# Optimization experiments

Hardware: AMD Instinct MI355X
Metric: run time of the kernel (lower is better)

The kernel has to match this reference:

```python
import jax, jax.numpy as jnp
import numpy as np

VOCAB = 100000
SHORTLIST = 10000  # cutoffs = [10000, 20000, 40000, 80000], n_clusters = 4
B, T, D = 1024, 128, 1024


def setup_inputs() -> dict:
    key = jax.random.key(0)
    ks = jax.random.split(key, 12)
    s = 0.02  # realistic init scale for weights
    inp = {
        "features": jax.random.normal(ks[0], (B, D), jnp.float32),
        "head_weight": jax.random.normal(ks[1], (SHORTLIST + 4, D), jnp.float32) * s,
        "proj0": jax.random.normal(ks[2], (512, D), jnp.float32) * s,
        "out0": jax.random.normal(ks[3], (10000, 512), jnp.float32) * s,
        "proj1": jax.random.normal(ks[4], (256, D), jnp.float32) * s,
        "out1": jax.random.normal(ks[5], (20000, 256), jnp.float32) * s,
        "proj2": jax.random.normal(ks[6], (128, D), jnp.float32) * s,
        "out2": jax.random.normal(ks[7], (40000, 128), jnp.float32) * s,
        "proj3": jax.random.normal(ks[8], (64, D), jnp.float32) * s,
        "out3": jax.random.normal(ks[9], (20000, 64), jnp.float32) * s,
        "discard_probs": jax.random.uniform(ks[10], (VOCAB,), jnp.float32),
        "targets": jax.random.randint(ks[11], (B, T), 0, VOCAB, jnp.int64),
        "target_mask": jnp.ones((B, T), jnp.bool_),
    }
    return inp


def _adaptive_log_prob(x, head_weight, projs, outs):
    # head: shortlist logits + one logit per tail cluster
    head_lp = jax.nn.log_softmax(x @ head_weight.T, axis=-1)  # [B, SHORTLIST+4]
    parts = [head_lp[:, :SHORTLIST]]
    for i, (pw, ow) in enumerate(zip(projs, outs)):
        cluster_logits = (x @ pw.T) @ ow.T  # [B, osz]
        parts.append(jax.nn.log_softmax(cluster_logits, axis=-1)
                     + head_lp[:, SHORTLIST + i:SHORTLIST + i + 1])
    return jnp.concatenate(parts, axis=-1)  # [B, VOCAB]


def reference(features, head_weight, proj0, out0, proj1, out1, proj2, out2,
              proj3, out3, discard_probs, targets, target_mask):
    # dropout is identity in eval/reference mode
    logprob = _adaptive_log_prob(features, head_weight,
                                 (proj0, proj1, proj2, proj3),
                                 (out0, out1, out2, out3))
    lp_t = jnp.take_along_axis(logprob, targets, axis=1)        # [B, T]
    w = (1.0 - discard_probs[targets]) * target_mask.astype(lp_t.dtype)
    per_sample = jnp.sum(-lp_t * w, axis=1) / jnp.sum(w, axis=1)  # [B]
    return jnp.sum(per_sample) / (targets.shape[0] + 1e-5)
```

## Files before the change

kernel.cpp:

```cpp
#include <hip/hip_runtime.h>
#include <cstdint>


typedef unsigned short u16;
typedef __attribute__((ext_vector_type(4))) float f32x4;
typedef __attribute__((ext_vector_type(8))) __bf16 bf16x8;
typedef __attribute__((ext_vector_type(4))) unsigned int u32x4;

__device__ __forceinline__ u16 f2bf(float f){
  unsigned u = __float_as_uint(f);
  u += 0x7FFFu + ((u >> 16) & 1u);
  return (u16)(u >> 16);
}

__device__ __forceinline__ void load_lds16(const void* g, void* l){
  __builtin_amdgcn_global_load_lds(
      (__attribute__((address_space(1))) void*)(uintptr_t)g,
      (__attribute__((address_space(3))) void*)(unsigned)(uintptr_t)l,
      16, 0, 0);
}

__device__ __forceinline__ float wave_sum(float v){
  #pragma unroll
  for (int d = 1; d < 64; d <<= 1) v += __shfl_xor(v, d, 64);
  return v;
}

__device__ __forceinline__ float wave_dot(const u16* a, const u16* b, int len, int lane){
  float s = 0.f;
  for (int k = lane*8; k < len; k += 512){
    u32x4 va = *(const u32x4*)(a + k);
    u32x4 vb = *(const u32x4*)(b + k);
    #pragma unroll
    for (int i = 0; i < 4; i++){
      unsigned ua = va[i], ub = vb[i];
      s = fmaf(__uint_as_float(ua << 16),        __uint_as_float(ub << 16),        s);
      s = fmaf(__uint_as_float(ua & 0xFFFF0000u), __uint_as_float(ub & 0xFFFF0000u), s);
    }
  }
  return wave_sum(s);
}

struct CvtSeg { const float* src; u16* dst; unsigned start; };
struct CvtTab { CvtSeg s[10]; unsigned total; };

__global__ __launch_bounds__(256) void cvt_bf16(CvtTab t){
  unsigned stride = gridDim.x * blockDim.x;
  for (unsigned c = blockIdx.x*blockDim.x + threadIdx.x; c < t.total; c += stride){
    int si = 0;
    #pragma unroll
    for (int i = 1; i < 10; i++) if (c >= t.s[i].start) si = i;
    unsigned lo = c - t.s[si].start;
    const float4* sp = (const float4*)t.s[si].src + (size_t)lo*2;
    float4 f0 = sp[0], f1 = sp[1];
    uint4 d;
    d.x = (unsigned)f2bf(f0.x) | ((unsigned)f2bf(f0.y) << 16);
    d.y = (unsigned)f2bf(f0.z) | ((unsigned)f2bf(f0.w) << 16);
    d.z = (unsigned)f2bf(f1.x) | ((unsigned)f2bf(f1.y) << 16);
    d.w = (unsigned)f2bf(f1.z) | ((unsigned)f2bf(f1.w) << 16);
    ((uint4*)t.s[si].dst)[lo] = d;
  }
}

struct GemmSeg {
  const u16* A; const u16* B; float* part; u16* C; float* gates;
  int lda, N, K, ntiles, tileStart, ldc;
};
struct GemmTab { GemmSeg seg[5]; int nseg; };

__global__ __launch_bounds__(256) void gemm_ms(GemmTab tab){
  __shared__ u16 ldsA[128*64];
  __shared__ u16 ldsB[128*64];
  __shared__ float msLds[128][2];

  int bx = blockIdx.y;
  int s = 0;
  #pragma unroll
  for (int i = 1; i < 5; i++)
    if (i < tab.nseg && bx >= tab.seg[i].tileStart) s = i;
  const u16* Ab = tab.seg[s].A;
  const u16* Bb = tab.seg[s].B;
  float* part = tab.seg[s].part;
  u16* Cc = tab.seg[s].C;
  float* gatesp = tab.seg[s].gates;
  int lda = tab.seg[s].lda, N = tab.seg[s].N, K = tab.seg[s].K;
  int ntiles = tab.seg[s].ntiles, ldc = tab.seg[s].ldc;
  int tileN = bx - tab.seg[s].tileStart;
  int row0 = blockIdx.x * 128;
  int n0 = tileN * 128;

  int tid = threadIdx.x;
  int wid = tid >> 6, lane = tid & 63;
  int wr = wid >> 1, wc = wid & 1;
  int qr = lane >> 4, ln = lane & 15;

  f32x4 acc[4][4];
  const f32x4 zero = {0.f, 0.f, 0.f, 0.f};
  #pragma unroll
  for (int i = 0; i < 4; i++)
    #pragma unroll
    for (int j = 0; j < 4; j++) acc[i][j] = zero;

  int rr_[4], kcs_[4];
  #pragma unroll
  for (int j = 0; j < 4; j++){
    int c = (wid*4 + j)*64 + lane;
    rr_[j]  = c >> 3;
    kcs_[j] = (c & 7) ^ (rr_[j] & 7);
  }

  int nkt = K >> 6;
  for (int kt = 0; kt < nkt; kt++){
    int kbase = kt * 64;
    #pragma unroll
    for (int j = 0; j < 4; j++){
      const u16* g = Ab + (size_t)(row0 + rr_[j])*lda + kbase + kcs_[j]*8;
      load_lds16(g, (char*)ldsA + (size_t)(wid*4 + j)*1024);
    }
    #pragma unroll
    for (int j = 0; j < 4; j++){
      int nr = n0 + rr_[j]; if (nr >= N) nr = N - 1;
      const u16* g = Bb + (size_t)nr*K + kbase + kcs_[j]*8;
      load_lds16(g, (char*)ldsB + (size_t)(wid*4 + j)*1024);
    }
    __syncthreads();
    #pragma unroll
    for (int ks = 0; ks < 2; ks++){
      bf16x8 av[4], bv[4];
      #pragma unroll
      for (int mt = 0; mt < 4; mt++){
        int rl = wr*64 + mt*16 + ln;
        int ch = rl*8 + ((ks*4 + qr) ^ (rl & 7));
        av[mt] = *(const bf16x8*)((const char*)ldsA + ch*16);
      }
      #pragma unroll
      for (int nt = 0; nt < 4; nt++){
        int rl = wc*64 + nt*16 + ln;
        int ch = rl*8 + ((ks*4 + qr) ^ (rl & 7));
        bv[nt] = *(const bf16x8*)((const char*)ldsB + ch*16);
      }
      #pragma unroll
      for (int mt = 0; mt < 4; mt++)
        #pragma unroll
        for (int nt = 0; nt < 4; nt++)
          acc[mt][nt] = __builtin_amdgcn_mfma_f32_16x16x32_bf16(av[mt], bv[nt], acc[mt][nt], 0, 0, 0);
    }
    __syncthreads();
  }

  if (part){
    #pragma unroll
    for (int mt = 0; mt < 4; mt++){
      #pragma unroll
      for (int r = 0; r < 4; r++){
        float ss = 0.f;
        #pragma unroll
        for (int nt = 0; nt < 4; nt++){
          int col = n0 + wc*64 + nt*16 + ln;
          if (col < N){
            float v = acc[mt][nt][r];
            ss += __expf(v);
            if (gatesp && col >= 10000){
              int row = row0 + wr*64 + mt*16 + qr*4 + r;
              gatesp[row*4 + (col - 10000)] = v;
            }
          }
        }
        ss += __shfl_xor(ss, 1, 64);
        ss += __shfl_xor(ss, 2, 64);
        ss += __shfl_xor(ss, 4, 64);
        ss += __shfl_xor(ss, 8, 64);
        if (ln == 0) msLds[wr*64 + mt*16 + qr*4 + r][wc] = ss;
      }
    }
    __syncthreads();
    if (tid < 128)
      part[(size_t)(row0 + tid)*ntiles + tileN] = msLds[tid][0] + msLds[tid][1];
  } else {
    #pragma unroll
    for (int mt = 0; mt < 4; mt++)
      #pragma unroll
      for (int nt = 0; nt < 4; nt++)
        #pragma unroll
        for (int r = 0; r < 4; r++){
          int col = n0 + wc*64 + nt*16 + ln;
          if (col < N){
            int row = row0 + wr*64 + mt*16 + qr*4 + r;
            Cc[(size_t)row*ldc + col] = f2bf(acc[mt][nt][r]);
          }
        }
  }
}

template<int K, int MLOOP>
__global__ __launch_bounds__(256) void gemm_bres(const u16* __restrict__ A,
    const u16* __restrict__ B, float* __restrict__ part,
    int lda, int N, int ntiles){
  constexpr int KC = K/8;
  __shared__ u16 ldsB[128*K];
  __shared__ u16 ldsA[128*64];
  float* msLds = (float*)ldsA;

  int tid = threadIdx.x;
  int wid = tid >> 6, lane = tid & 63;
  int wr = wid >> 1, wc = wid & 1;
  int qr = lane >> 4, ln = lane & 15;
  int tileN = blockIdx.x;
  int n0 = tileN * 128;

  #pragma unroll
  for (int j = 0; j < KC/2; j++){
    int p = (wid*(KC/2) + j)*64 + lane;
    int row = p / KC;
    int jj  = p % KC;
    int nr = n0 + row; if (nr >= N) nr = N - 1;
    const u16* g = B + (size_t)nr*K + (size_t)(jj ^ (row & 7))*8;
    load_lds16(g, (char*)ldsB + (size_t)(wid*(KC/2) + j)*1024);
  }

  for (int m = 0; m < MLOOP; m++){
    int mbase = (blockIdx.y*MLOOP + m)*128;
    f32x4 acc[4][4];
    const f32x4 zero = {0.f, 0.f, 0.f, 0.f};
    #pragma unroll
    for (int i = 0; i < 4; i++)
      #pragma unroll
      for (int j = 0; j < 4; j++) acc[i][j] = zero;

    #pragma unroll
    for (int kt = 0; kt < K/64; kt++){
      #pragma unroll
      for (int j = 0; j < 4; j++){
        int p = (wid*4 + j)*64 + lane;
        int row = p >> 3, jj = p & 7;
        const u16* g = A + (size_t)(mbase + row)*lda + kt*64 + (jj ^ (row & 7))*8;
        load_lds16(g, (char*)ldsA + (size_t)(wid*4 + j)*1024);
      }
      __syncthreads();
      #pragma unroll
      for (int ks = 0; ks < 2; ks++){
        bf16x8 av[4], bv[4];
        #pragma unroll
        for (int mt = 0; mt < 4; mt++){
          int rl = wr*64 + mt*16 + ln;
          int ch = rl*8 + ((ks*4 + qr) ^ (rl & 7));
          av[mt] = *(const bf16x8*)((const char*)ldsA + ch*16);
        }
        #pragma unroll
        for (int nt = 0; nt < 4; nt++){
          int rl = wc*64 + nt*16 + ln;
          int kg = kt*8 + ks*4 + qr;
          int ch = rl*KC + (kg ^ (rl & 7));
          bv[nt] = *(const bf16x8*)((const char*)ldsB + ch*16);
        }
        #pragma unroll
        for (int mt = 0; mt < 4; mt++)
          #pragma unroll
          for (int nt = 0; nt < 4; nt++)
            acc[mt][nt] = __builtin_amdgcn_mfma_f32_16x16x32_bf16(av[mt], bv[nt], acc[mt][nt], 0, 0, 0);
      }
      __syncthreads();
    }

    #pragma unroll
    for (int mt = 0; mt < 4; mt++){
      #pragma unroll
      for (int r = 0; r < 4; r++){
        float ss = 0.f;
        #pragma unroll
        for (int nt = 0; nt < 4; nt++){
          int col = n0 + wc*64 + nt*16 + ln;
          if (col < N) ss += __expf(acc[mt][nt][r]);
        }
        ss += __shfl_xor(ss, 1, 64);
        ss += __shfl_xor(ss, 2, 64);
        ss += __shfl_xor(ss, 4, 64);
        ss += __shfl_xor(ss, 8, 64);
        if (ln == 0) msLds[(wr*64 + mt*16 + qr*4 + r)*2 + wc] = ss;
      }
    }
    __syncthreads();
    if (tid < 128)
      part[(size_t)(mbase + tid)*ntiles + tileN] = msLds[tid*2] + msLds[tid*2 + 1];
    __syncthreads();
  }
}

struct LseTab { const float* base[5]; int ntiles[5]; float* lse; };

__global__ __launch_bounds__(256) void lse_reduce(LseTab t){
  int widx = blockIdx.x*4 + (threadIdx.x >> 6);
  int lane = threadIdx.x & 63;
  int mat = widx >> 10, row = widx & 1023;
  const float* p = t.base[mat] + (size_t)row * t.ntiles[mat];
  float s = 0.f;
  for (int i = lane; i < t.ntiles[mat]; i += 64) s += p[i];
  s = wave_sum(s);
  if (lane == 0) t.lse[mat*1024 + row] = __logf(s);
}

struct GatherArgs {
  const u16* Xb; const u16* Hb; const u16* Hact; const u16* Ob;
  const float* lse; const float* gates; const int* targets; float* lp;
};

__global__ __launch_bounds__(256) void gather_k(GatherArgs g){
  int idx = blockIdx.x*4 + (threadIdx.x >> 6);
  int lane = threadIdx.x & 63;
  int v = g.targets[idx];
  int b = idx >> 7;
  float val;
  if (v < 10000){
    float logit = wave_dot(g.Xb + (size_t)b*1024, g.Hb + (size_t)v*1024, 1024, lane);
    val = logit - g.lse[b];
  } else {
    int c, off, psz, hoff; size_t oboff;
    if      (v < 20000){ c=0; off=10000; psz=512; hoff=0;   oboff=0; }
    else if (v < 40000){ c=1; off=20000; psz=256; hoff=512; oboff=5120000; }
    else if (v < 80000){ c=2; off=40000; psz=128; hoff=768; oboff=10240000; }
    else               { c=3; off=80000; psz=64;  hoff=896; oboff=15360000; }
    float logit = wave_dot(g.Hact + (size_t)b*960 + hoff,
                           g.Ob + oboff + (size_t)(v - off)*psz, psz, lane);
    val = g.gates[b*4 + c] - g.lse[b] + logit - g.lse[(c+1)*1024 + b];
  }
  if (lane == 0) g.lp[idx] = val;
}

__global__ __launch_bounds__(128) void row_loss(const float* lp, const int* targets,
                                                const float* discard, float* psamp){
  int b = blockIdx.x, t = threadIdx.x;
  int idx = b*128 + t;
  int v = targets[idx];
  float w = 1.0f - discard[v];
  float a = -lp[idx] * w;
  float as = wave_sum(a), ws = wave_sum(w);
  __shared__ float sa[2], sw[2];
  int wid = t >> 6, lane = t & 63;
  if (lane == 0){ sa[wid] = as; sw[wid] = ws; }
  __syncthreads();
  if (t == 0) psamp[b] = (sa[0] + sa[1]) / (sw[0] + sw[1]);
}

__global__ __launch_bounds__(256) void final_sum(const float* psamp, float* out){
  float s = 0.f;
  for (int i = threadIdx.x; i < 1024; i += 256) s += psamp[i];
  s = wave_sum(s);
  __shared__ float sb[4];
  if ((threadIdx.x & 63) == 0) sb[threadIdx.x >> 6] = s;
  __syncthreads();
  if (threadIdx.x == 0) out[0] = (sb[0] + sb[1] + sb[2] + sb[3]) / (1024.0f + 1e-5f);
}

extern "C" void kernel_launch(void* const* d_in, const int* in_sizes, int n_in,
                              void* d_out, int out_size, void* d_ws, size_t ws_size,
                              hipStream_t stream){
  (void)in_sizes; (void)n_in; (void)out_size; (void)ws_size;
  const float* features = (const float*)d_in[0];
  const float* head_w   = (const float*)d_in[1];
  const float* proj[4]  = {(const float*)d_in[2], (const float*)d_in[4],
                           (const float*)d_in[6], (const float*)d_in[8]};
  const float* outw[4]  = {(const float*)d_in[3], (const float*)d_in[5],
                           (const float*)d_in[7], (const float*)d_in[9]};
  const float* discard  = (const float*)d_in[10];
  const int*   targets  = (const int*)d_in[11];
  float* out = (float*)d_out;

  char* wsp = (char*)d_ws;
  size_t off = 0;
  auto carve = [&](size_t bytes)->char*{
    char* p = wsp + off; off += (bytes + 255) & ~(size_t)255; return p;
  };
  u16* Xb     = (u16*)carve(1024ull*1024*2);
  u16* Hb     = (u16*)carve(10004ull*1024*2);
  u16* Pb     = (u16*)carve(960ull*1024*2);
  u16* Ob     = (u16*)carve(16640000ull*2);
  u16* Hact   = (u16*)carve(1024ull*960*2);
  float* part = (float*)carve(803840ull*4);
  float* lse  = (float*)carve(5*1024*4);
  float* gates= (float*)carve(4096*4);
  float* lp   = (float*)carve(131072ull*4);
  float* psamp= (float*)carve(1024*4);

  CvtTab ct{};
  const float* srcs[10] = {features, head_w, proj[0], proj[1], proj[2], proj[3],
                           outw[0], outw[1], outw[2], outw[3]};
  u16* dsts[10] = {Xb, Hb, Pb, Pb + 512*1024, Pb + 768*1024, Pb + 896*1024,
                   Ob, Ob + 5120000, Ob + 10240000, Ob + 15360000};
  unsigned counts[10] = {1048576u, 10244096u, 524288u, 262144u, 131072u, 65536u,
                         5120000u, 5120000u, 5120000u, 1280000u};
  unsigned pre = 0;
  for (int i = 0; i < 10; i++){
    ct.s[i].src = srcs[i]; ct.s[i].dst = dsts[i]; ct.s[i].start = pre;
    pre += counts[i] / 8;
  }
  ct.total = pre;
  cvt_bf16<<<dim3(4096), dim3(256), 0, stream>>>(ct);

  float* pHead = part;
  float* pC0 = part + 80896;
  float* pC1 = part + 161792;
  float* pC2 = part + 322560;
  float* pC3 = part + 643072;

  GemmTab t1{};
  t1.nseg = 5;
  t1.seg[0] = {Xb, Hb,            pHead,   nullptr,    gates,   1024, 10004, 1024, 79, 0,  0};
  t1.seg[1] = {Xb, Pb,            nullptr, Hact,       nullptr, 1024, 512,   1024, 4,  79, 960};
  t1.seg[2] = {Xb, Pb + 512*1024, nullptr, Hact + 512, nullptr, 1024, 256,   1024, 2,  83, 960};
  t1.seg[3] = {Xb, Pb + 768*1024, nullptr, Hact + 768, nullptr, 1024, 128,   1024, 1,  85, 960};
  t1.seg[4] = {Xb, Pb + 896*1024, nullptr, Hact + 896, nullptr, 1024, 64,    1024, 1,  86, 960};
  gemm_ms<<<dim3(8, 87), dim3(256), 0, stream>>>(t1);

  GemmTab t2{};
  t2.nseg = 1;
  t2.seg[0] = {Hact, Ob, pC0, nullptr, nullptr, 960, 10000, 512, 79, 0, 0};
  gemm_ms<<<dim3(8, 79), dim3(256), 0, stream>>>(t2);

  gemm_bres<256,2><<<dim3(157, 4), dim3(256), 0, stream>>>(
      Hact + 512, Ob + 5120000, pC1, 960, 20000, 157);
  gemm_bres<128,2><<<dim3(313, 4), dim3(256), 0, stream>>>(
      Hact + 768, Ob + 10240000, pC2, 960, 40000, 313);
  gemm_bres<64,2><<<dim3(157, 4), dim3(256), 0, stream>>>(
      Hact + 896, Ob + 15360000, pC3, 960, 20000, 157);

  LseTab lt{};
  lt.base[0] = pHead; lt.base[1] = pC0; lt.base[2] = pC1; lt.base[3] = pC2; lt.base[4] = pC3;
  lt.ntiles[0] = 79; lt.ntiles[1] = 79; lt.ntiles[2] = 157; lt.ntiles[3] = 313; lt.ntiles[4] = 157;
  lt.lse = lse;
  lse_reduce<<<dim3(1280), dim3(256), 0, stream>>>(lt);

  GatherArgs ga{Xb, Hb, Hact, Ob, lse, gates, targets, lp};
  gather_k<<<dim3(32768), dim3(256), 0, stream>>>(ga);

  row_loss<<<dim3(1024), dim3(128), 0, stream>>>(lp, targets, discard, psamp);
  final_sum<<<dim3(1), dim3(256), 0, stream>>>(psamp, out);
}
```

Before: 361.3 us.

## Replace gemm_ms with register-prefetched 256x128 tile GEMM for head and cluster0

The multi-segment GEMM now uses 256x128 tiles, with each wave owning 64 rows across all 128 columns. Global loads for the next K step are prefetched into registers while MFMAs run on the current LDS tile, replacing the synchronous global_load_lds path. The larger tile halves the number of row blocks and cuts reloads of B. It also drops the cross-wave LDS reduction, so each wave writes its partial sum directly. The cost is more registers (a 4x8 accumulator plus prefetch buffers, with launch bounds of 2), fewer blocks in the grid, and a wider epilogue.

```diff
diff --git a/kernel.cpp b/kernel.cpp
--- a/kernel.cpp
+++ b/kernel.cpp
@@ -62,90 +62,98 @@
   }
 }
 
-struct GemmSeg {
-  const u16* A; const u16* B; float* part; u16* C; float* gates;
-  int lda, N, K, ntiles, tileStart, ldc;
-};
-struct GemmTab { GemmSeg seg[5]; int nseg; };
-
-__global__ __launch_bounds__(256) void gemm_ms(GemmTab tab){
-  __shared__ u16 ldsA[128*64];
+struct PSeg { const u16* B; float* part; u16* C; float* gates;
+              int N, K, ntiles, tileStart, ldc; };
+struct PTab { const u16* A; int lda; PSeg seg[5]; int nseg; };
+
+__global__ __launch_bounds__(256, 2) void gemm_pipe(PTab tab){
+  __shared__ u16 ldsA[256*64];
   __shared__ u16 ldsB[128*64];
-  __shared__ float msLds[128][2];
-
-  int bx = blockIdx.y;
+
+  int by = blockIdx.y;
   int s = 0;
   #pragma unroll
   for (int i = 1; i < 5; i++)
-    if (i < tab.nseg && bx >= tab.seg[i].tileStart) s = i;
-  const u16* Ab = tab.seg[s].A;
+    if (i < tab.nseg && by >= tab.seg[i].tileStart) s = i;
   const u16* Bb = tab.seg[s].B;
-  float* part = tab.seg[s].part;
-  u16* Cc = tab.seg[s].C;
+  float* part   = tab.seg[s].part;
+  u16* Cc       = tab.seg[s].C;
   float* gatesp = tab.seg[s].gates;
-  int lda = tab.seg[s].lda, N = tab.seg[s].N, K = tab.seg[s].K;
+  int N = tab.seg[s].N, K = tab.seg[s].K;
   int ntiles = tab.seg[s].ntiles, ldc = tab.seg[s].ldc;
-  int tileN = bx - tab.seg[s].tileStart;
-  int row0 = blockIdx.x * 128;
+  int tileN = by - tab.seg[s].tileStart;
   int n0 = tileN * 128;
+  int row0 = blockIdx.x * 256;
+  int lda = tab.lda;
 
   int tid = threadIdx.x;
-  int wid = tid >> 6, lane = tid & 63;
-  int wr = wid >> 1, wc = wid & 1;
+  int w = tid >> 6, lane = tid & 63;
   int qr = lane >> 4, ln = lane & 15;
 
-  f32x4 acc[4][4];
+  const char* baseA = (const char*)(tab.A + (size_t)row0*lda);
+  const char* baseB = (const char*)Bb;
+  unsigned offA[8], offB[4];
+  #pragma unroll
+  for (int t = 0; t < 8; t++){
+    int c = t*256 + tid, row = c >> 3, jj = (c & 7) ^ (row & 7);
+    offA[t] = (unsigned)(row*lda + jj*8) * 2u;
+  }
+  #pragma unroll
+  for (int t = 0; t < 4; t++){
+    int c = t*256 + tid, row = c >> 3, jj = (c & 7) ^ (row & 7);
+    int nr = n0 + row; if (nr >= N) nr = N - 1;
+    offB[t] = (unsigned)(nr*K + jj*8) * 2u;
+  }
+
+  u32x4 pa[8], pb[4];
+  #pragma unroll
+  for (int t = 0; t < 8; t++) pa[t] = *(const u32x4*)(baseA + offA[t]);
+  #pragma unroll
+  for (int t = 0; t < 4; t++) pb[t] = *(const u32x4*)(baseB + offB[t]);
+
+  f32x4 acc[4][8];
   const f32x4 zero = {0.f, 0.f, 0.f, 0.f};
   #pragma unroll
   for (int i = 0; i < 4; i++)
     #pragma unroll
-    for (int j = 0; j < 4; j++) acc[i][j] = zero;
-
-  int rr_[4], kcs_[4];
-  #pragma unroll
-  for (int j = 0; j < 4; j++){
-    int c = (wid*4 + j)*64 + lane;
-    rr_[j]  = c >> 3;
-    kcs_[j] = (c & 7) ^ (rr_[j] & 7);
-  }
+    for (int j = 0; j < 8; j++) acc[i][j] = zero;
 
   int nkt = K >> 6;
   for (int kt = 0; kt < nkt; kt++){
-    int kbase = kt * 64;
-    #pragma unroll
-    for (int j = 0; j < 4; j++){
-      const u16* g = Ab + (size_t)(row0 + rr_[j])*lda + kbase + kcs_[j]*8;
-      load_lds16(g, (char*)ldsA + (size_t)(wid*4 + j)*1024);
-    }
-    #pragma unroll
-    for (int j = 0; j < 4; j++){
-      int nr = n0 + rr_[j]; if (nr >= N) nr = N - 1;
-      const u16* g = Bb + (size_t)nr*K + kbase + kcs_[j]*8;
-      load_lds16(g, (char*)ldsB + (size_t)(wid*4 + j)*1024);
-    }
     __syncthreads();
     #pragma unroll
+    for (int t = 0; t < 8; t++)
+      *(u32x4*)((char*)ldsA + (size_t)(t*256 + tid)*16) = pa[t];
+    #pragma unroll
+    for (int t = 0; t < 4; t++)
+      *(u32x4*)((char*)ldsB + (size_t)(t*256 + tid)*16) = pb[t];
+    __syncthreads();
+    if (kt + 1 < nkt){
+      unsigned kb = (unsigned)(kt + 1) * 128u;
+      #pragma unroll
+      for (int t = 0; t < 8; t++) pa[t] = *(const u32x4*)(baseA + offA[t] + kb);
+      #pragma unroll
+      for (int t = 0; t < 4; t++) pb[t] = *(const u32x4*)(baseB + offB[t] + kb);
+    }
+    #pragma unroll
     for (int ks = 0; ks < 2; ks++){
-      bf16x8 av[4], bv[4];
+      bf16x8 av[4];
       #pragma unroll
       for (int mt = 0; mt < 4; mt++){
-        int rl = wr*64 + mt*16 + ln;
+        int rl = w*64 + mt*16 + ln;
         int ch = rl*8 + ((ks*4 + qr) ^ (rl & 7));
         av[mt] = *(const bf16x8*)((const char*)ldsA + ch*16);
       }
       #pragma unroll
-      for (int nt = 0; nt < 4; nt++){
-        int rl = wc*64 + nt*16 + ln;
+      for (int nt = 0; nt < 8; nt++){
+        int rl = nt*16 + ln;
         int ch = rl*8 + ((ks*4 + qr) ^ (rl & 7));
-        bv[nt] = *(const bf16x8*)((const char*)ldsB + ch*16);
-      }
-      #pragma unroll
-      for (int mt = 0; mt < 4; mt++)
-        #pragma unroll
-        for (int nt = 0; nt < 4; nt++)
-          acc[mt][nt] = __builtin_amdgcn_mfma_f32_16x16x32_bf16(av[mt], bv[nt], acc[mt][nt], 0, 0, 0);
-    }
-    __syncthreads();
+        bf16x8 bv = *(const bf16x8*)((const char*)ldsB + ch*16);
+        #pragma unroll
+        for (int mt = 0; mt < 4; mt++)
+          acc[mt][nt] = __builtin_amdgcn_mfma_f32_16x16x32_bf16(av[mt], bv, acc[mt][nt], 0, 0, 0);
+      }
+    }
   }
 
   if (part){
@@ -155,13 +163,13 @@
       for (int r = 0; r < 4; r++){
         float ss = 0.f;
         #pragma unroll
-        for (int nt = 0; nt < 4; nt++){
-          int col = n0 + wc*64 + nt*16 + ln;
+        for (int nt = 0; nt < 8; nt++){
+          int col = n0 + nt*16 + ln;
           if (col < N){
             float v = acc[mt][nt][r];
             ss += __expf(v);
             if (gatesp && col >= 10000){
-              int row = row0 + wr*64 + mt*16 + qr*4 + r;
+              int row = row0 + w*64 + mt*16 + qr*4 + r;
               gatesp[row*4 + (col - 10000)] = v;
             }
           }
@@ -170,22 +178,22 @@
         ss += __shfl_xor(ss, 2, 64);
         ss += __shfl_xor(ss, 4, 64);
         ss += __shfl_xor(ss, 8, 64);
-        if (ln == 0) msLds[wr*64 + mt*16 + qr*4 + r][wc] = ss;
-      }
-    }
-    __syncthreads();
-    if (tid < 128)
-      part[(size_t)(row0 + tid)*ntiles + tileN] = msLds[tid][0] + msLds[tid][1];
+        if (ln == 0){
+          int row = row0 + w*64 + mt*16 + qr*4 + r;
+          part[(size_t)row*ntiles + tileN] = ss;
+        }
+      }
+    }
   } else {
     #pragma unroll
     for (int mt = 0; mt < 4; mt++)
       #pragma unroll
-      for (int nt = 0; nt < 4; nt++)
+      for (int nt = 0; nt < 8; nt++)
         #pragma unroll
         for (int r = 0; r < 4; r++){
-          int col = n0 + wc*64 + nt*16 + ln;
+          int col = n0 + nt*16 + ln;
           if (col < N){
-            int row = row0 + wr*64 + mt*16 + qr*4 + r;
+            int row = row0 + w*64 + mt*16 + qr*4 + r;
             Cc[(size_t)row*ldc + col] = f2bf(acc[mt][nt][r]);
           }
         }
@@ -402,19 +410,19 @@
   float* pC2 = part + 322560;
   float* pC3 = part + 643072;
 
-  GemmTab t1{};
-  t1.nseg = 5;
-  t1.seg[0] = {Xb, Hb,            pHead,   nullptr,    gates,   1024, 10004, 1024, 79, 0,  0};
-  t1.seg[1] = {Xb, Pb,            nullptr, Hact,       nullptr, 1024, 512,   1024, 4,  79, 960};
-  t1.seg[2] = {Xb, Pb + 512*1024, nullptr, Hact + 512, nullptr, 1024, 256,   1024, 2,  83, 960};
-  t1.seg[3] = {Xb, Pb + 768*1024, nullptr, Hact + 768, nullptr, 1024, 128,   1024, 1,  85, 960};
-  t1.seg[4] = {Xb, Pb + 896*1024, nullptr, Hact + 896, nullptr, 1024, 64,    1024, 1,  86, 960};
-  gemm_ms<<<dim3(8, 87), dim3(256), 0, stream>>>(t1);
-
-  GemmTab t2{};
-  t2.nseg = 1;
-  t2.seg[0] = {Hact, Ob, pC0, nullptr, nullptr, 960, 10000, 512, 79, 0, 0};
-  gemm_ms<<<dim3(8, 79), dim3(256), 0, stream>>>(t2);
+  PTab t1{};
+  t1.A = Xb; t1.lda = 1024; t1.nseg = 5;
+  t1.seg[0] = {Hb,            pHead,   nullptr,    gates,   10004, 1024, 79, 0,  0};
+  t1.seg[1] = {Pb,            nullptr, Hact,       nullptr, 512,   1024, 4,  79, 960};
+  t1.seg[2] = {Pb + 512*1024, nullptr, Hact + 512, nullptr, 256,   1024, 2,  83, 960};
+  t1.seg[3] = {Pb + 768*1024, nullptr, Hact + 768, nullptr, 128,   1024, 1,  85, 960};
+  t1.seg[4] = {Pb + 896*1024, nullptr, Hact + 896, nullptr, 64,    1024, 1,  86, 960};
+  gemm_pipe<<<dim3(4, 87), dim3(256), 0, stream>>>(t1);
+
+  PTab t2{};
+  t2.A = Hact; t2.lda = 960; t2.nseg = 1;
+  t2.seg[0] = {Ob, pC0, nullptr, nullptr, 10000, 512, 79, 0, 0};
+  gemm_pipe<<<dim3(4, 79), dim3(256), 0, stream>>>(t2);
 
   gemm_bres<256,2><<<dim3(157, 4), dim3(256), 0, stream>>>(
       Hact + 512, Ob + 5120000, pC1, 960, 20000, 157);
```

Result: faster. 346.4 us (-4.1%).
